# Performance work log

Measured on AMD Instinct MI355X. Metric: run time of the kernel, lower is better.

## Reference

```python
import jax, jax.numpy as jnp
import numpy as np

D_MODEL = 1024
N, L = 4, 2048


def setup_inputs() -> dict:
    key = jax.random.key(0)
    ks = jax.random.split(key, 8)
    s = 0.1
    return {
        "X": jax.random.normal(ks[0], (N, L, D_MODEL), dtype=jnp.float32),
        "W_Q1": jax.random.normal(ks[1], (D_MODEL, D_MODEL), dtype=jnp.float32) * s,
        "W_K1": jax.random.normal(ks[2], (D_MODEL, D_MODEL), dtype=jnp.float32) * s,
        "W_V1": jax.random.normal(ks[3], (D_MODEL, D_MODEL), dtype=jnp.float32) * s,
        "W_Q2": jax.random.normal(ks[4], (D_MODEL, D_MODEL), dtype=jnp.float32) * s,
        "W_K2": jax.random.normal(ks[5], (D_MODEL, D_MODEL), dtype=jnp.float32) * s,
        "W_V2": jax.random.normal(ks[6], (D_MODEL, D_MODEL), dtype=jnp.float32) * s,
        "W_O": jax.random.normal(ks[7], (D_MODEL, 1), dtype=jnp.float32) * s,
        "b_O": jnp.zeros((1, 1), dtype=jnp.float32),
    }


def _attn_block(H, W_Q, W_K, W_V):
    # H: (N, L, D); single-head scaled dot-product attention
    Q = jnp.einsum('nld,dk->nlk', H, W_Q)
    K = jnp.einsum('nld,dk->nlk', H, W_K)
    V = jnp.einsum('nld,dk->nlk', H, W_V)
    scale = jnp.sqrt(jnp.asarray(Q.shape[-1], Q.dtype))
    scores = jnp.einsum('nqd,nkd->nqk', Q, K) / scale  # (N, L, L)
    attn = jax.nn.softmax(scores, axis=-1)
    return jnp.einsum('nqk,nkd->nqd', attn, V)


def reference(X, W_Q1, W_K1, W_V1, W_Q2, W_K2, W_V2, W_O, b_O):
    H1 = _attn_block(X, W_Q1, W_K1, W_V1)
    H2 = _attn_block(H1, W_Q2, W_K2, W_V2)
    pooled = jnp.mean(H2, axis=1)            # (N, D)
    logits = pooled @ W_O + b_O              # (N, 1)
    return jax.nn.sigmoid(logits).squeeze(-1)  # (N,)
```

## Files before the change

kernel.cpp:

```cpp
#include <hip/hip_runtime.h>
#include <hip/hip_bf16.h>
#include <cstdint>


#define DEVFN __device__ __forceinline__

typedef __attribute__((ext_vector_type(8))) short bf16x8;
typedef __attribute__((ext_vector_type(4))) float f32x4;
typedef unsigned short u16;

DEVFN u16 f2bf(float f) {
    uint32_t x = __float_as_uint(f);
    x += 0x7fffu + ((x >> 16) & 1u);
    return (u16)(x >> 16);
}
DEVFN float bf2f(u16 u) { return __uint_as_float(((uint32_t)u) << 16); }

DEVFN void gload_lds16(const void* g, void* l) {
    __builtin_amdgcn_global_load_lds(
        (const __attribute__((address_space(1))) void*)g,
        (__attribute__((address_space(3))) void*)l, 16, 0, 0);
}

#define MFMA16 __builtin_amdgcn_mfma_f32_16x16x32_bf16

template<int EPI>
__global__ __launch_bounds__(256, 4) void gemmk(
    const u16* __restrict__ A, long long aStride,
    const u16* __restrict__ B, long long bStride,
    void* __restrict__ out0, void* __restrict__ out1,
    const float* __restrict__ zrow, long long cStride,
    int M, int N, int K, int lda, int ldb, int ldc, float scale)
{
    constexpr int ASEC  = 128 * 32;
    constexpr int BUFSZ = ASEC + 128 * 32;
    constexpr int NU    = 4;

    __shared__ __align__(16) u16 L[2 * BUFSZ];
    const int tid  = threadIdx.x;
    const int wave = tid >> 6, lane = tid & 63;

    const int gx = gridDim.x, gy = gridDim.y;
    const int nwg = gx * gy * gridDim.z;
    int flat = (blockIdx.z * gy + blockIdx.y) * gx + blockIdx.x;
    flat = (flat & 7) * (nwg >> 3) + (flat >> 3);
    const int bx = flat % gx, by = (flat / gx) % gy, bz = flat / (gx * gy);

    const u16* pA = A + (size_t)bz * aStride;
    const u16* pB = B + (size_t)bz * bStride;
    const int m0 = by * 128, n0 = bx * 128;

    const u16* src[NU];
    int dst[NU];
#pragma unroll
    for (int q = 0; q < 2; q++) {
        const int s = q * 256 + tid, row = s >> 2, c = (s & 3) ^ ((row >> 1) & 3);
        src[q]     = pA + (size_t)(m0 + row) * lda + c * 8;
        dst[q]     = q * 2048 + wave * 512;
        src[2 + q] = pB + (size_t)(n0 + row) * ldb + c * 8;
        dst[2 + q] = ASEC + q * 2048 + wave * 512;
    }

    const int fr = lane & 15, ch = lane >> 4;
    const int wr = (wave >> 1) * 64, wc = (wave & 1) * 64;

    const int NT = K >> 5;

#pragma unroll
    for (int u = 0; u < NU; u++) { gload_lds16(src[u], &L[dst[u]]); src[u] += 32; }
    __syncthreads();

    f32x4 acc[4][4] = {};
    int cur = 0;

    for (int kt = 0; kt < NT; ++kt) {
        const int cOff = cur * BUFSZ;
        const int sOff = BUFSZ - cOff;
        if (kt + 1 < NT) {
#pragma unroll
            for (int u = 0; u < NU; u++) { gload_lds16(src[u], &L[sOff + dst[u]]); src[u] += 32; }
        }

        bf16x8 ah[4], bh[4];
#pragma unroll
        for (int i = 0; i < 4; i++) {
            const int r = wr + i * 16 + fr;
            ah[i] = *(const bf16x8*)&L[cOff + r * 32 + ((ch ^ ((r >> 1) & 3)) << 3)];
        }
#pragma unroll
        for (int j = 0; j < 4; j++) {
            const int r = wc + j * 16 + fr;
            bh[j] = *(const bf16x8*)&L[cOff + ASEC + r * 32 + ((ch ^ ((r >> 1) & 3)) << 3)];
        }

#pragma unroll
        for (int i = 0; i < 4; i++)
#pragma unroll
            for (int j = 0; j < 4; j++)
                acc[i][j] = MFMA16(ah[i], bh[j], acc[i][j], 0, 0, 0);

        __syncthreads();
        cur ^= 1;
    }

    if constexpr (EPI == 5) {
#pragma unroll
        for (int i = 0; i < 4; i++)
#pragma unroll
            for (int r = 0; r < 4; r++) {
                const int rowb = m0 + wr + i * 16 + ch * 4 + r;
                float s = 0.f;
#pragma unroll
                for (int j = 0; j < 4; j++) {
                    const int col = n0 + wc + j * 16 + fr;
                    const float e = __expf(acc[i][j][r] * scale - 60.f);
                    s += e;
                    ((u16*)out0)[(size_t)bz * cStride + (size_t)rowb * ldc + col] = f2bf(e);
                }
                s += __shfl_xor(s, 1, 16);
                s += __shfl_xor(s, 2, 16);
                s += __shfl_xor(s, 4, 16);
                s += __shfl_xor(s, 8, 16);
                if (fr == 0)
                    ((float*)out1)[((size_t)bz * 2048 + rowb) * 32 + ((n0 + wc) >> 6)] = s;
            }
    } else if constexpr (EPI == 6) {
#pragma unroll
        for (int i = 0; i < 4; i++)
#pragma unroll
            for (int r = 0; r < 4; r++) {
                const int row = m0 + wr + i * 16 + ch * 4 + r;
                const size_t grow = (size_t)bz * 2048 + row;
                float zp = zrow[grow * 32 + 2 * fr] + zrow[grow * 32 + 2 * fr + 1];
                zp += __shfl_xor(zp, 1, 16);
                zp += __shfl_xor(zp, 2, 16);
                zp += __shfl_xor(zp, 4, 16);
                zp += __shfl_xor(zp, 8, 16);
                const float zi = 1.f / zp;
#pragma unroll
                for (int j = 0; j < 4; j++) {
                    const int col = n0 + wc + j * 16 + fr;
                    ((u16*)out0)[(size_t)bz * cStride + (size_t)row * ldc + col] =
                        f2bf(acc[i][j][r] * zi);
                }
            }
    } else {
#pragma unroll
        for (int i = 0; i < 4; i++)
#pragma unroll
            for (int j = 0; j < 4; j++)
#pragma unroll
                for (int r = 0; r < 4; r++) {
                    const int row = m0 + wr + i * 16 + (lane >> 4) * 4 + r;
                    const int col = n0 + wc + j * 16 + (lane & 15);
                    const float v = acc[i][j][r] * scale;
                    if constexpr (EPI == 1) {
                        ((float*)out0)[(size_t)bz * cStride + (size_t)row * ldc + col] = v;
                    } else {
                        ((u16*)out0)[(size_t)bz * cStride + (size_t)row * ldc + col] = f2bf(v);
                    }
                }
    }
}

__global__ __launch_bounds__(256) void prep_all(
    const float* __restrict__ X,
    const float* __restrict__ W0, const float* __restrict__ W1,
    const float* __restrict__ W2, const float* __restrict__ W3,
    const float* __restrict__ Wv1, const float* __restrict__ Wv2,
    const float* __restrict__ wO,
    u16* __restrict__ Xb, u16* __restrict__ Wcat,
    u16* __restrict__ Wv1T, float* __restrict__ wv)
{
    const int blk = blockIdx.x, tid = threadIdx.x;
    __shared__ float t[64][65];

    if (blk < 8192) {
        const size_t i = ((size_t)blk * 256 + tid) * 4;
        const float4 v = *(const float4*)&X[i];
        ushort4 h;
        h.x = f2bf(v.x); h.y = f2bf(v.y); h.z = f2bf(v.z); h.w = f2bf(v.w);
        *(ushort4*)&Xb[i] = h;
    } else if (blk < 12288) {
        const int w = (blk - 8192) >> 10, ib = (blk - 8192) & 1023;
        const float* W = (w == 0) ? W0 : (w == 1) ? W1 : (w == 2) ? W2 : W3;
        u16* o = Wcat + (size_t)w * 1048576;
        const size_t i = ((size_t)ib * 256 + tid) * 4;
        const float4 v = *(const float4*)&W[i];
        ushort4 h;
        h.x = f2bf(v.x); h.y = f2bf(v.y); h.z = f2bf(v.z); h.w = f2bf(v.w);
        *(ushort4*)&o[i] = h;
    } else if (blk < 12544) {
        const int tb = blk - 12288;
        const int r0 = (tb >> 4) * 64, c0 = (tb & 15) * 64;
#pragma unroll
        for (int it = 0; it < 16; it++) {
            const int idx = it * 256 + tid, rr = idx >> 6, cc = idx & 63;
            t[rr][cc] = Wv1[(size_t)(r0 + rr) * 1024 + (c0 + cc)];
        }
        __syncthreads();
#pragma unroll
        for (int it = 0; it < 16; it++) {
            const int idx = it * 256 + tid, nn = idx >> 6, kk = idx & 63;
            Wv1T[(size_t)(c0 + nn) * 1024 + (r0 + kk)] = f2bf(t[kk][nn]);
        }
    } else {
        const int d = (blk - 12544) * 16 + (tid >> 4);
        const int lx = tid & 15;
        const float* row = Wv2 + (size_t)d * 1024;
        float s = 0.f;
#pragma unroll
        for (int it = 0; it < 16; it++) {
            const int j = it * 64 + lx * 4;
            const float4 a = *(const float4*)&row[j];
            const float4 w = *(const float4*)&wO[j];
            s += a.x * w.x + a.y * w.y + a.z * w.z + a.w * w.w;
        }
#pragma unroll
        for (int o = 8; o; o >>= 1) s += __shfl_xor(s, o, 16);
        if (lx == 0) wv[d] = s;
    }
}

__global__ __launch_bounds__(256) void softmax_colsum(
    const float* __restrict__ S, float* __restrict__ part)
{
    const int b = blockIdx.x, chunk = blockIdx.y;
    const int tid = threadIdx.x;
    const float* Sb = S + (size_t)b * (2048 * 2048) + (size_t)chunk * 16 * 2048;
    __shared__ float redm[4], reds[4];
    float acc[8] = {};

    for (int r = 0; r < 16; r++) {
        const float* row = Sb + (size_t)r * 2048;
        const float4 a = *(const float4*)&row[tid * 8];
        const float4 bb = *(const float4*)&row[tid * 8 + 4];
        float v[8] = {a.x, a.y, a.z, a.w, bb.x, bb.y, bb.z, bb.w};

        float m = v[0];
#pragma unroll
        for (int j = 1; j < 8; j++) m = fmaxf(m, v[j]);
        for (int o = 32; o; o >>= 1) m = fmaxf(m, __shfl_xor(m, o));
        if ((tid & 63) == 0) redm[tid >> 6] = m;
        __syncthreads();
        m = fmaxf(fmaxf(redm[0], redm[1]), fmaxf(redm[2], redm[3]));

        float e[8], s = 0.f;
#pragma unroll
        for (int j = 0; j < 8; j++) { e[j] = __expf(v[j] - m); s += e[j]; }
        for (int o = 32; o; o >>= 1) s += __shfl_xor(s, o);
        if ((tid & 63) == 0) reds[tid >> 6] = s;
        __syncthreads();
        const float inv = 1.f / (reds[0] + reds[1] + reds[2] + reds[3]);
#pragma unroll
        for (int j = 0; j < 8; j++) acc[j] += e[j] * inv;
        __syncthreads();
    }

    float* p = part + ((size_t)(b * 128 + chunk)) * 2048;
#pragma unroll
    for (int j = 0; j < 8; j++) p[tid * 8 + j] = acc[j];
}

__global__ __launch_bounds__(256) void colsum_reduce(
    const float* __restrict__ part, float* __restrict__ csum)
{
    const int b = blockIdx.x;
    const int kl = threadIdx.x & 63;
    const int k = blockIdx.y * 64 + kl;
    const int cg = threadIdx.x >> 6;
    float s = 0.f;
#pragma unroll 4
    for (int c = 0; c < 32; c++)
        s += part[((size_t)(b * 128 + cg * 32 + c)) * 2048 + k];
    __shared__ float red[4][64];
    red[cg][kl] = s;
    __syncthreads();
    if (cg == 0)
        csum[b * 2048 + k] = red[0][kl] + red[1][kl] + red[2][kl] + red[3][kl];
}

__global__ __launch_bounds__(256) void u_dot(
    const u16* __restrict__ H1, const float* __restrict__ wv,
    float* __restrict__ u)
{
    const int r = blockIdx.x * 16 + (threadIdx.x >> 4);
    const int lx = threadIdx.x & 15;
    const u16* row = H1 + (size_t)r * 1024;
    float s = 0.f;
#pragma unroll
    for (int it = 0; it < 8; it++) {
        const int d = it * 128 + lx * 8;
        const bf16x8 h = *(const bf16x8*)&row[d];
#pragma unroll
        for (int j = 0; j < 8; j++) s += bf2f((u16)h[j]) * wv[d + j];
    }
#pragma unroll
    for (int o = 8; o; o >>= 1) s += __shfl_xor(s, o, 16);
    if (lx == 0) u[r] = s;
}

__global__ void head_final(const float* __restrict__ csum,
                           const float* __restrict__ u,
                           const float* __restrict__ bO, float* __restrict__ out)
{
    const int b = threadIdx.x >> 6, lane = threadIdx.x & 63;
    float s = 0.f;
    for (int k = lane; k < 2048; k += 64)
        s += csum[b * 2048 + k] * u[b * 2048 + k];
    for (int o = 32; o; o >>= 1) s += __shfl_xor(s, o);
    if (lane == 0) {
        const float logit = s * (1.f / 2048.f) + bO[0];
        out[b] = 1.f / (1.f + __expf(-logit));
    }
}

extern "C" void kernel_launch(void* const* d_in, const int* in_sizes, int n_in,
                              void* d_out, int out_size, void* d_ws, size_t ws_size,
                              hipStream_t stream)
{
    const float* X   = (const float*)d_in[0];
    const float* Wq1 = (const float*)d_in[1];
    const float* Wk1 = (const float*)d_in[2];
    const float* Wv1 = (const float*)d_in[3];
    const float* Wq2 = (const float*)d_in[4];
    const float* Wk2 = (const float*)d_in[5];
    const float* Wv2 = (const float*)d_in[6];
    const float* WO  = (const float*)d_in[7];
    const float* bO  = (const float*)d_in[8];
    float* out = (float*)d_out;

    uint8_t* ws = (uint8_t*)d_ws;
    const size_t MB = 1ull << 20;
    u16* Xb   = (u16*)(ws + 0);
    u16* Tb   = (u16*)(ws + 32 * MB);
    float* part  = (float*)(ws + 80 * MB);
    float* csum  = (float*)(ws + 85 * MB);
    float* wv    = (float*)(ws + 86 * MB);
    float* ud    = (float*)(ws + 87 * MB);
    float* Zpart = (float*)(ws + 88 * MB);
    u16* Vtb  = (u16*)(ws + 96 * MB);
    u16* Wcat = (u16*)(ws + 128 * MB);
    u16* Eb   = (u16*)(ws + 152 * MB);
    float* S  = (float*)(ws + 152 * MB);

    auto Wslot = [&](int i) { return Wcat + (size_t)i * 1048576; };

    prep_all<<<12608, 256, 0, stream>>>(
        X, Wq1, Wq2, Wk1, Wk2, Wv1, Wv2, WO, Xb, Wcat, Wslot(5), wv);
    gemmk<3><<<dim3(8, 8, 2), 256, 0, stream>>>(
        Wslot(2), 1048576, Wslot(0), 1048576, Wslot(4), nullptr, nullptr,
        2 * 1048576LL, 1024, 1024, 1024, 1024, 1024, 1024, 1.f);

    const long long LD2 = 2048LL * 1024;
    const long long EST = 2048LL * 2048;
    const long long SST = 2048LL * 2048;

    gemmk<3><<<dim3(8, 64, 1), 256, 0, stream>>>(
        Xb, 0, Wslot(4), 0, Tb, nullptr, nullptr, 0,
        8192, 1024, 1024, 1024, 1024, 1024, 1.f);
    gemmk<3><<<dim3(64, 8, 1), 256, 0, stream>>>(
        Wslot(5), 0, Xb, 0, Vtb, nullptr, nullptr, 0,
        1024, 8192, 1024, 1024, 1024, 8192, 1.f);
    gemmk<5><<<dim3(16, 16, 4), 256, 0, stream>>>(
        Tb, LD2, Xb, LD2, Eb, Zpart, nullptr, EST,
        2048, 2048, 1024, 1024, 1024, 2048, 0.03125f);
    gemmk<6><<<dim3(8, 16, 4), 256, 0, stream>>>(
        Eb, EST, Vtb, 2048, Xb, nullptr, Zpart, LD2,
        2048, 1024, 2048, 2048, 8192, 1024, 1.f);

    gemmk<3><<<dim3(8, 64, 1), 256, 0, stream>>>(
        Xb, 0, Wslot(6), 0, Tb, nullptr, nullptr, 0,
        8192, 1024, 1024, 1024, 1024, 1024, 1.f);
    gemmk<1><<<dim3(16, 16, 4), 256, 0, stream>>>(
        Tb, LD2, Xb, LD2, S, nullptr, nullptr, SST,
        2048, 2048, 1024, 1024, 1024, 2048, 0.03125f);

    softmax_colsum<<<dim3(4, 128), 256, 0, stream>>>(S, part);
    colsum_reduce<<<dim3(4, 32), 256, 0, stream>>>(part, csum);
    u_dot<<<512, 256, 0, stream>>>(Xb, wv, ud);
    head_final<<<1, 256, 0, stream>>>(csum, ud, bO, out);
}
```

Measured before the change: 277.7 us.

## Store second-block scores as fp16 and merge tail reduction kernels

The second attention block's score matrix is now written by the GEMM epilogue as fp16 instead of fp32, and softmax_colsum reads it back with 8-wide half loads. This halves the score traffic in both the write and the read of a 64 MB-class intermediate. The colsum reduction and u_dot kernels are merged into one launch to save launch overhead. The risk is lost precision and possible fp16 overflow in the scaled scores before the softmax.

```diff
diff --git a/kernel.cpp b/kernel.cpp
--- a/kernel.cpp
+++ b/kernel.cpp
@@ -6,6 +6,7 @@
 #define DEVFN __device__ __forceinline__
 
 typedef __attribute__((ext_vector_type(8))) short bf16x8;
+typedef __attribute__((ext_vector_type(8))) _Float16 f16x8;
 typedef __attribute__((ext_vector_type(4))) float f32x4;
 typedef unsigned short u16;
 
@@ -154,10 +155,11 @@
                     const int row = m0 + wr + i * 16 + (lane >> 4) * 4 + r;
                     const int col = n0 + wc + j * 16 + (lane & 15);
                     const float v = acc[i][j][r] * scale;
-                    if constexpr (EPI == 1) {
-                        ((float*)out0)[(size_t)bz * cStride + (size_t)row * ldc + col] = v;
+                    if constexpr (EPI == 3) {
+                        ((u16*)out0)[(size_t)bz * cStride + (size_t)row * ldc + col] = f2bf(v);
                     } else {
-                        ((u16*)out0)[(size_t)bz * cStride + (size_t)row * ldc + col] = f2bf(v);
+                        ((_Float16*)out0)[(size_t)bz * cStride + (size_t)row * ldc + col] =
+                            (_Float16)v;
                     }
                 }
     }
@@ -223,19 +225,20 @@
 }
 
 __global__ __launch_bounds__(256) void softmax_colsum(
-    const float* __restrict__ S, float* __restrict__ part)
+    const _Float16* __restrict__ S, float* __restrict__ part)
 {
     const int b = blockIdx.x, chunk = blockIdx.y;
     const int tid = threadIdx.x;
-    const float* Sb = S + (size_t)b * (2048 * 2048) + (size_t)chunk * 16 * 2048;
+    const _Float16* Sb = S + (size_t)b * (2048 * 2048) + (size_t)chunk * 16 * 2048;
     __shared__ float redm[4], reds[4];
     float acc[8] = {};
 
     for (int r = 0; r < 16; r++) {
-        const float* row = Sb + (size_t)r * 2048;
-        const float4 a = *(const float4*)&row[tid * 8];
-        const float4 bb = *(const float4*)&row[tid * 8 + 4];
-        float v[8] = {a.x, a.y, a.z, a.w, bb.x, bb.y, bb.z, bb.w};
+        const _Float16* row = Sb + (size_t)r * 2048;
+        const f16x8 hv = *(const f16x8*)&row[tid * 8];
+        float v[8];
+#pragma unroll
+        for (int j = 0; j < 8; j++) v[j] = (float)hv[j];
 
         float m = v[0];
 #pragma unroll
@@ -262,42 +265,42 @@
     for (int j = 0; j < 8; j++) p[tid * 8 + j] = acc[j];
 }
 
-__global__ __launch_bounds__(256) void colsum_reduce(
-    const float* __restrict__ part, float* __restrict__ csum)
-{
-    const int b = blockIdx.x;
-    const int kl = threadIdx.x & 63;
-    const int k = blockIdx.y * 64 + kl;
-    const int cg = threadIdx.x >> 6;
-    float s = 0.f;
-#pragma unroll 4
-    for (int c = 0; c < 32; c++)
-        s += part[((size_t)(b * 128 + cg * 32 + c)) * 2048 + k];
-    __shared__ float red[4][64];
-    red[cg][kl] = s;
-    __syncthreads();
-    if (cg == 0)
-        csum[b * 2048 + k] = red[0][kl] + red[1][kl] + red[2][kl] + red[3][kl];
-}
-
-__global__ __launch_bounds__(256) void u_dot(
+__global__ __launch_bounds__(256) void tail_reduce(
+    const float* __restrict__ part, float* __restrict__ csum,
     const u16* __restrict__ H1, const float* __restrict__ wv,
     float* __restrict__ u)
 {
-    const int r = blockIdx.x * 16 + (threadIdx.x >> 4);
-    const int lx = threadIdx.x & 15;
-    const u16* row = H1 + (size_t)r * 1024;
-    float s = 0.f;
-#pragma unroll
-    for (int it = 0; it < 8; it++) {
-        const int d = it * 128 + lx * 8;
-        const bf16x8 h = *(const bf16x8*)&row[d];
-#pragma unroll
-        for (int j = 0; j < 8; j++) s += bf2f((u16)h[j]) * wv[d + j];
-    }
-#pragma unroll
-    for (int o = 8; o; o >>= 1) s += __shfl_xor(s, o, 16);
-    if (lx == 0) u[r] = s;
+    const int blk = blockIdx.x, tid = threadIdx.x;
+    if (blk < 128) {
+        const int b = blk >> 5;
+        const int kl = tid & 63;
+        const int k = (blk & 31) * 64 + kl;
+        const int cg = tid >> 6;
+        float s = 0.f;
+#pragma unroll 4
+        for (int c = 0; c < 32; c++)
+            s += part[((size_t)(b * 128 + cg * 32 + c)) * 2048 + k];
+        __shared__ float red[4][64];
+        red[cg][kl] = s;
+        __syncthreads();
+        if (cg == 0)
+            csum[b * 2048 + k] = red[0][kl] + red[1][kl] + red[2][kl] + red[3][kl];
+    } else {
+        const int r = (blk - 128) * 16 + (tid >> 4);
+        const int lx = tid & 15;
+        const u16* row = H1 + (size_t)r * 1024;
+        float s = 0.f;
+#pragma unroll
+        for (int it = 0; it < 8; it++) {
+            const int d = it * 128 + lx * 8;
+            const bf16x8 h = *(const bf16x8*)&row[d];
+#pragma unroll
+            for (int j = 0; j < 8; j++) s += bf2f((u16)h[j]) * wv[d + j];
+        }
+#pragma unroll
+        for (int o = 8; o; o >>= 1) s += __shfl_xor(s, o, 16);
+        if (lx == 0) u[r] = s;
+    }
 }
 
 __global__ void head_final(const float* __restrict__ csum,
@@ -342,7 +345,7 @@
     u16* Vtb  = (u16*)(ws + 96 * MB);
     u16* Wcat = (u16*)(ws + 128 * MB);
     u16* Eb   = (u16*)(ws + 152 * MB);
-    float* S  = (float*)(ws + 152 * MB);
+    _Float16* Sh = (_Float16*)(ws + 152 * MB);
 
     auto Wslot = [&](int i) { return Wcat + (size_t)i * 1048576; };
 
@@ -354,7 +357,6 @@
 
     const long long LD2 = 2048LL * 1024;
     const long long EST = 2048LL * 2048;
-    const long long SST = 2048LL * 2048;
 
     gemmk<3><<<dim3(8, 64, 1), 256, 0, stream>>>(
         Xb, 0, Wslot(4), 0, Tb, nullptr, nullptr, 0,
@@ -372,12 +374,11 @@
     gemmk<3><<<dim3(8, 64, 1), 256, 0, stream>>>(
         Xb, 0, Wslot(6), 0, Tb, nullptr, nullptr, 0,
         8192, 1024, 1024, 1024, 1024, 1024, 1.f);
-    gemmk<1><<<dim3(16, 16, 4), 256, 0, stream>>>(
-        Tb, LD2, Xb, LD2, S, nullptr, nullptr, SST,
+    gemmk<8><<<dim3(16, 16, 4), 256, 0, stream>>>(
+        Tb, LD2, Xb, LD2, Sh, nullptr, nullptr, EST,
         2048, 2048, 1024, 1024, 1024, 2048, 0.03125f);
 
-    softmax_colsum<<<dim3(4, 128), 256, 0, stream>>>(S, part);
-    colsum_reduce<<<dim3(4, 32), 256, 0, stream>>>(part, csum);
-    u_dot<<<512, 256, 0, stream>>>(Xb, wv, ud);
+    softmax_colsum<<<dim3(4, 128), 256, 0, stream>>>(Sh, part);
+    tail_reduce<<<640, 256, 0, stream>>>(part, csum, Xb, wv, ud);
     head_final<<<1, 256, 0, stream>>>(csum, ud, bO, out);
 }
```

Measured after the change: 273.0 us. No clear change (-1.7%).
